# Kernel optimization log

Hardware: AMD Instinct MI355X
Metric: run time of the kernel (lower is better)

The kernel has to match this reference:

```python
import math
import jax, jax.numpy as jnp
import numpy as np

NUM_GAUSSIANS = 1024
WIDTH = 256
HEIGHT = 256
BG_COLOR = (0.0, 0.0, 0.0)
JITTER = 1e-6


def setup_inputs() -> dict:
    key = jax.random.key(0)
    k1, k2, k3 = jax.random.split(key, 3)
    means = jax.random.normal(k1, (NUM_GAUSSIANS, 2), dtype=jnp.float32)
    # init: randn - e (keeps exp(scales) small)
    scales = jax.random.normal(k2, (NUM_GAUSSIANS, 2), dtype=jnp.float32) - math.e
    thetas = jax.random.normal(k3, (NUM_GAUSSIANS, 1), dtype=jnp.float32)
    # init: inverse_sigmoid(0.1) with eps=1e-5
    eps = 1e-5
    inv_sig = math.log((0.1 + eps) / (1.0 - 0.1 + eps))
    opacities = jnp.full((NUM_GAUSSIANS, 1), inv_sig, dtype=jnp.float32)
    return {"means": means, "scales": scales, "thetas": thetas, "opacities": opacities}


def reference(means, scales, thetas, opacities):
    # activations
    m = jnp.tanh(means)                       # [N,2] in [-1,1]
    s = jnp.exp(scales)                       # [N,2]
    th = jax.nn.sigmoid(thetas[:, 0]) * 2.0 * jnp.pi  # [N]
    op = jax.nn.sigmoid(opacities[:, 0])      # [N]

    # covariance = R diag(s^2) R^T + jitter*I, 2x2, closed form
    c, si = jnp.cos(th), jnp.sin(th)
    s2 = s * s
    a = c * c * s2[:, 0] + si * si * s2[:, 1] + JITTER   # Sigma_00
    b = c * si * (s2[:, 0] - s2[:, 1])                    # Sigma_01
    d = si * si * s2[:, 0] + c * c * s2[:, 1] + JITTER   # Sigma_11
    det = a * d - b * b
    ia, ib, id_ = d / det, -b / det, a / det              # Sigma^{-1}

    # pixel grid over [-1,1]^2
    xs = jnp.linspace(-1.0, 1.0, WIDTH, dtype=jnp.float32)
    ys = jnp.linspace(-1.0, 1.0, HEIGHT, dtype=jnp.float32)
    X, Y = jnp.meshgrid(xs, ys)               # [H,W]

    dx = X[None] - m[:, 0, None, None]        # [N,H,W]
    dy = Y[None] - m[:, 1, None, None]        # [N,H,W]
    q = (ia[:, None, None] * dx * dx
         + 2.0 * ib[:, None, None] * dx * dy
         + id_[:, None, None] * dy * dy)      # Mahalanobis dist^2
    alpha = op[:, None, None] * jnp.exp(-0.5 * q)  # [N,H,W]

    # front-to-back alpha compositing in gaussian index order
    T = jnp.cumprod(1.0 - alpha, axis=0)      # transmittance after each gaussian
    T_excl = jnp.concatenate([jnp.ones((1, HEIGHT, WIDTH), jnp.float32), T[:-1]], axis=0)
    acc = jnp.sum(alpha * T_excl, axis=0)     # [H,W], white splats

    bg = jnp.asarray(BG_COLOR, dtype=jnp.float32)
    image = acc[..., None] + T[-1][..., None] * bg   # [H,W,3]
    return image
```

## Files before the change

kernel.cpp:

```cpp
#include <hip/hip_runtime.h>
#include <math.h>

#define NG 1024
#define NWAVES 4
#define IMG_W 256
#define IMG_H 256
#define TILE 8
#define JITTER 1e-6f
#define L2E 1.4426950408889634f
#define CULL_LOG2_EPS -20.0f

__device__ __forceinline__ float fexp2(float x)  { return __builtin_amdgcn_exp2f(x); }
__device__ __forceinline__ float flog2(float x)  { return __builtin_amdgcn_logf(x); }
__device__ __forceinline__ float frcp(float x)   { return __builtin_amdgcn_rcpf(x); }
__device__ __forceinline__ float fsqrt(float x)  { return __builtin_amdgcn_sqrtf(x); }
__device__ __forceinline__ float fexp(float x)   { return fexp2(x * L2E); }
__device__ __forceinline__ float fsigmoid(float x) { return frcp(1.0f + fexp(-x)); }
__device__ __forceinline__ float ftanh(float x) {
    float t = fexp2(2.0f * L2E * x);
    return 1.0f - 2.0f * frcp(t + 1.0f);
}

__global__ __launch_bounds__(256, 4)
void gs_tiled(const float* __restrict__ means,
              const float* __restrict__ scales,
              const float* __restrict__ thetas,
              const float* __restrict__ opacities,
              float* __restrict__ out) {
    __shared__ float4 s_c0123[NG];
    __shared__ float2 s_c45[NG];
    __shared__ unsigned long long s_mask[4][NWAVES];
    __shared__ float2 s_seg[NWAVES][64];

    int tid  = threadIdx.x;
    int lane = tid & 63;
    int wave = tid >> 6;

    const float step = 2.0f / 255.0f;
    int tx = blockIdx.x & (IMG_W / TILE - 1);
    int ty = blockIdx.x >> 5;
    float rx0 = fmaf((float)(tx * TILE), step, -1.0f);
    float ry0 = fmaf((float)(ty * TILE), step, -1.0f);
    float rx1 = rx0 + (TILE - 1) * step;
    float ry1 = ry0 + (TILE - 1) * step;

    int nsurv = 0;
    for (int k = 0; k < 4; ++k) {
        int g = k * 256 + tid;
        float mx = ftanh(means[2 * g]);
        float my = ftanh(means[2 * g + 1]);
        float s2x = fexp(2.0f * scales[2 * g]);
        float s2y = fexp(2.0f * scales[2 * g + 1]);
        float rev = fsigmoid(thetas[g]);
        float si = __builtin_amdgcn_sinf(rev);
        float c  = __builtin_amdgcn_cosf(rev);
        float a = c * c * s2x + si * si * s2y + JITTER;
        float b = c * si * (s2x - s2y);
        float d = si * si * s2x + c * c * s2y + JITTER;
        float inv_det = frcp(a * d - b * b);
        float P = -0.5f * L2E * d * inv_det;
        float Q =  L2E * b * inv_det;
        float R = -0.5f * L2E * a * inv_det;
        float l2op = flog2(fsigmoid(opacities[g]));
        float c3 = P, c4 = Q, c5 = R;
        float c1 = -(2.0f * P * mx + Q * my);
        float c2 = -(Q * mx + 2.0f * R * my);
        float c0 = P * mx * mx + Q * mx * my + R * my * my + l2op;

        float lam = 0.5f * ((a + d) + fsqrt((a - d) * (a - d) + 4.0f * b * b));
        float Kc = 0.5f * L2E * frcp(lam);
        float ddx = fmaxf(fmaxf(rx0 - mx, mx - rx1), 0.0f);
        float ddy = fmaxf(fmaxf(ry0 - my, my - ry1), 0.0f);
        float d2 = ddx * ddx + ddy * ddy;
        bool keep = (l2op - Kc * d2) >= CULL_LOG2_EPS;

        unsigned long long bal = __ballot(keep);
        if (lane == 0) s_mask[k][wave] = bal;
        __syncthreads();

        int pos = nsurv;
        #pragma unroll
        for (int w = 0; w < NWAVES; ++w) {
            unsigned long long m = s_mask[k][w];
            if (w < wave) pos += __popcll(m);
            nsurv += __popcll(m);
        }
        pos += __popcll(bal & ((1ull << lane) - 1ull));

        if (keep) {
            s_c0123[pos] = make_float4(c0, c1, c2, c3);
            s_c45[pos]   = make_float2(c4, c5);
        }
        __syncthreads();
    }

    int Ns = nsurv;
    int sbeg = __builtin_amdgcn_readfirstlane((Ns * wave) >> 2);
    int send = __builtin_amdgcn_readfirstlane((Ns * (wave + 1)) >> 2);

    float x = fmaf((float)(lane & 7), step, rx0);
    float y = fmaf((float)(lane >> 3), step, ry0);
    float xx = x * x, xy = x * y, yy = y * y;

    float acc = 0.0f, T = 1.0f;
    #pragma unroll 4
    for (int i = sbeg; i < send; ++i) {
        float4 q = s_c0123[i];
        float2 r = s_c45[i];
        float e2 = fmaf(q.w, xx,
                   fmaf(r.x, xy,
                   fmaf(r.y, yy,
                   fmaf(q.y, x,
                   fmaf(q.z, y, q.x)))));
        float alpha = fexp2(e2);
        acc = fmaf(alpha, T, acc);
        T = fmaf(-alpha, T, T);
    }

    s_seg[wave][lane] = make_float2(acc, T);
    __syncthreads();

    if (tid < 64) {
        float A = 0.0f, Tt = 1.0f;
        #pragma unroll
        for (int s = 0; s < NWAVES; ++s) {
            float2 v = s_seg[s][tid];
            A = fmaf(Tt, v.x, A);
            Tt *= v.y;
        }
        int px = tx * TILE + (tid & 7);
        int py = ty * TILE + (tid >> 3);
        float* o = out + 3 * (py * IMG_W + px);
        o[0] = A;
        o[1] = A;
        o[2] = A;
    }
}

extern "C" void kernel_launch(void* const* d_in, const int* in_sizes, int n_in,
                              void* d_out, int out_size, void* d_ws, size_t ws_size,
                              hipStream_t stream) {
    const float* means     = (const float*)d_in[0];
    const float* scales    = (const float*)d_in[1];
    const float* thetas    = (const float*)d_in[2];
    const float* opacities = (const float*)d_in[3];
    float* out = (float*)d_out;

    gs_tiled<<<dim3((IMG_W / TILE) * (IMG_H / TILE)), dim3(256), 0, stream>>>(
        means, scales, thetas, opacities, out);
}
```

Before: 68.04 us.

## Use 16x16 tiles with 8 waves and four pixels per lane

```diff
diff --git a/kernel.cpp b/kernel.cpp
--- a/kernel.cpp
+++ b/kernel.cpp
@@ -2,10 +2,10 @@
 #include <math.h>
 
 #define NG 1024
-#define NWAVES 4
+#define NWAVES 8
 #define IMG_W 256
 #define IMG_H 256
-#define TILE 8
+#define TILE 16
 #define JITTER 1e-6f
 #define L2E 1.4426950408889634f
 #define CULL_LOG2_EPS -20.0f
@@ -21,7 +21,7 @@
     return 1.0f - 2.0f * frcp(t + 1.0f);
 }
 
-__global__ __launch_bounds__(256, 4)
+__global__ __launch_bounds__(512, 2)
 void gs_tiled(const float* __restrict__ means,
               const float* __restrict__ scales,
               const float* __restrict__ thetas,
@@ -29,8 +29,8 @@
               float* __restrict__ out) {
     __shared__ float4 s_c0123[NG];
     __shared__ float2 s_c45[NG];
-    __shared__ unsigned long long s_mask[4][NWAVES];
-    __shared__ float2 s_seg[NWAVES][64];
+    __shared__ unsigned long long s_mask[NWAVES];
+    __shared__ float2 s_seg[NWAVES][TILE * TILE];
 
     int tid  = threadIdx.x;
     int lane = tid & 63;
@@ -38,15 +38,16 @@
 
     const float step = 2.0f / 255.0f;
     int tx = blockIdx.x & (IMG_W / TILE - 1);
-    int ty = blockIdx.x >> 5;
+    int ty = blockIdx.x >> 4;
     float rx0 = fmaf((float)(tx * TILE), step, -1.0f);
     float ry0 = fmaf((float)(ty * TILE), step, -1.0f);
     float rx1 = rx0 + (TILE - 1) * step;
     float ry1 = ry0 + (TILE - 1) * step;
 
     int nsurv = 0;
-    for (int k = 0; k < 4; ++k) {
-        int g = k * 256 + tid;
+    #pragma unroll
+    for (int k = 0; k < 2; ++k) {
+        int g = k * 512 + tid;
         float mx = ftanh(means[2 * g]);
         float my = ftanh(means[2 * g + 1]);
         float s2x = fexp(2.0f * scales[2 * g]);
@@ -62,7 +63,6 @@
         float Q =  L2E * b * inv_det;
         float R = -0.5f * L2E * a * inv_det;
         float l2op = flog2(fsigmoid(opacities[g]));
-        float c3 = P, c4 = Q, c5 = R;
         float c1 = -(2.0f * P * mx + Q * my);
         float c2 = -(Q * mx + 2.0f * R * my);
         float c0 = P * mx * mx + Q * mx * my + R * my * my + l2op;
@@ -75,52 +75,65 @@
         bool keep = (l2op - Kc * d2) >= CULL_LOG2_EPS;
 
         unsigned long long bal = __ballot(keep);
-        if (lane == 0) s_mask[k][wave] = bal;
+        if (lane == 0) s_mask[wave] = bal;
         __syncthreads();
 
         int pos = nsurv;
         #pragma unroll
         for (int w = 0; w < NWAVES; ++w) {
-            unsigned long long m = s_mask[k][w];
+            unsigned long long m = s_mask[w];
             if (w < wave) pos += __popcll(m);
             nsurv += __popcll(m);
         }
         pos += __popcll(bal & ((1ull << lane) - 1ull));
 
         if (keep) {
-            s_c0123[pos] = make_float4(c0, c1, c2, c3);
-            s_c45[pos]   = make_float2(c4, c5);
+            s_c0123[pos] = make_float4(c0, c1, c2, P);
+            s_c45[pos]   = make_float2(Q, R);
         }
         __syncthreads();
     }
 
     int Ns = nsurv;
-    int sbeg = __builtin_amdgcn_readfirstlane((Ns * wave) >> 2);
-    int send = __builtin_amdgcn_readfirstlane((Ns * (wave + 1)) >> 2);
+    int sbeg = __builtin_amdgcn_readfirstlane((Ns * wave) >> 3);
+    int send = __builtin_amdgcn_readfirstlane((Ns * (wave + 1)) >> 3);
 
-    float x = fmaf((float)(lane & 7), step, rx0);
-    float y = fmaf((float)(lane >> 3), step, ry0);
-    float xx = x * x, xy = x * y, yy = y * y;
+    int col  = lane & 15;
+    int rowg = lane >> 4;
+    float x  = fmaf((float)col, step, rx0);
+    float y0 = fmaf((float)(rowg * 4 + 0), step, ry0);
+    float y1 = y0 + step;
+    float y2 = y1 + step;
+    float y3 = y2 + step;
 
-    float acc = 0.0f, T = 1.0f;
+    float acc0 = 0.f, T0 = 1.f, acc1 = 0.f, T1 = 1.f;
+    float acc2 = 0.f, T2 = 1.f, acc3 = 0.f, T3 = 1.f;
+
     #pragma unroll 4
     for (int i = sbeg; i < send; ++i) {
         float4 q = s_c0123[i];
         float2 r = s_c45[i];
-        float e2 = fmaf(q.w, xx,
-                   fmaf(r.x, xy,
-                   fmaf(r.y, yy,
-                   fmaf(q.y, x,
-                   fmaf(q.z, y, q.x)))));
-        float alpha = fexp2(e2);
-        acc = fmaf(alpha, T, acc);
-        T = fmaf(-alpha, T, T);
+        float t1 = fmaf(x, fmaf(q.w, x, q.y), q.x);
+        float u  = fmaf(r.x, x, q.z);
+        float e, al;
+        e = fmaf(y0, fmaf(r.y, y0, u), t1); al = fexp2(e);
+        acc0 = fmaf(al, T0, acc0); T0 = fmaf(-al, T0, T0);
+        e = fmaf(y1, fmaf(r.y, y1, u), t1); al = fexp2(e);
+        acc1 = fmaf(al, T1, acc1); T1 = fmaf(-al, T1, T1);
+        e = fmaf(y2, fmaf(r.y, y2, u), t1); al = fexp2(e);
+        acc2 = fmaf(al, T2, acc2); T2 = fmaf(-al, T2, T2);
+        e = fmaf(y3, fmaf(r.y, y3, u), t1); al = fexp2(e);
+        acc3 = fmaf(al, T3, acc3); T3 = fmaf(-al, T3, T3);
     }
 
-    s_seg[wave][lane] = make_float2(acc, T);
+    int pxb = (rowg * 4) * TILE + col;
+    s_seg[wave][pxb]            = make_float2(acc0, T0);
+    s_seg[wave][pxb + TILE]     = make_float2(acc1, T1);
+    s_seg[wave][pxb + 2 * TILE] = make_float2(acc2, T2);
+    s_seg[wave][pxb + 3 * TILE] = make_float2(acc3, T3);
     __syncthreads();
 
-    if (tid < 64) {
+    if (tid < TILE * TILE) {
         float A = 0.0f, Tt = 1.0f;
         #pragma unroll
         for (int s = 0; s < NWAVES; ++s) {
@@ -128,8 +141,8 @@
             A = fmaf(Tt, v.x, A);
             Tt *= v.y;
         }
-        int px = tx * TILE + (tid & 7);
-        int py = ty * TILE + (tid >> 3);
+        int px = tx * TILE + (tid & 15);
+        int py = ty * TILE + (tid >> 4);
         float* o = out + 3 * (py * IMG_W + px);
         o[0] = A;
         o[1] = A;
@@ -146,6 +159,6 @@
     const float* opacities = (const float*)d_in[3];
     float* out = (float*)d_out;
 
-    gs_tiled<<<dim3((IMG_W / TILE) * (IMG_H / TILE)), dim3(256), 0, stream>>>(
+    gs_tiled<<<dim3((IMG_W / TILE) * (IMG_H / TILE)), dim3(512), 0, stream>>>(
         means, scales, thetas, opacities, out);
 }
```

After: 65.08 us. 1.05x faster.
